# Optimization experiments

Measured on AMD Instinct MI355X. Metric: run time of the kernel, lower is better.

The kernel has to match this reference:

```python
import jax, jax.numpy as jnp
import numpy as np

B, M = 4, 4096          # events x points-per-event (row_splits are uniform)
N = B * M
IN_DIM, SPACE, PROP, K = 128, 4, 64, 32


def setup_inputs() -> dict:
    key = jax.random.key(0)
    k1, k2, k3, k4, k5 = jax.random.split(key, 5)
    x = jax.random.normal(k1, (N, IN_DIM), jnp.float32)
    row_splits = (jnp.arange(B + 1, dtype=jnp.int32) * M)
    s = 1.0 / np.sqrt(IN_DIM)
    Ws = jax.random.uniform(k2, (IN_DIM, SPACE), jnp.float32, -s, s)
    bs = jax.random.uniform(k3, (SPACE,), jnp.float32, -s, s)
    Wp = jax.random.uniform(k4, (IN_DIM, PROP), jnp.float32, -s, s)
    bp = jax.random.uniform(k5, (PROP,), jnp.float32, -s, s)
    return {"x": x, "Ws": Ws, "bs": bs, "Wp": Wp, "bp": bp, "row_splits": row_splits}


def _gravnet(x, Ws, bs, Wp, bp):
    space = x @ Ws + bs                      # [N, SPACE] learned coordinates
    prop = x @ Wp + bp                       # [N, PROP]  features to propagate
    sp = space.reshape(B, M, SPACE)
    pr = prop.reshape(B, M, PROP)
    # exact KNN within each event (row_splits segment): pairwise squared dists
    sq = jnp.sum(sp * sp, axis=-1)                         # [B, M]
    d2 = sq[:, :, None] + sq[:, None, :] - 2.0 * jnp.einsum("bms,bns->bmn", sp, sp)
    neg_vals, idx = jax.lax.top_k(-d2, K)                  # k smallest dists (incl. self)
    distsq = jnp.maximum(-neg_vals, 0.0)                   # [B, M, K]
    weights = jnp.exp(-10.0 * distsq)                      # [B, M, K]
    gathered = jax.vmap(lambda p, i: p[i])(pr, idx)        # [B, M, K, PROP]
    weighted = gathered * weights[..., None]
    fmean = jnp.mean(weighted, axis=2)                     # [B, M, PROP]
    fmax = jnp.max(weighted, axis=2)                       # [B, M, PROP]
    out = jnp.concatenate([fmean, fmax], axis=-1)          # [B, M, 2*PROP]
    return out.reshape(N, 2 * PROP)


def reference(x, Ws, bs, Wp, bp, row_splits):
    # row_splits encodes uniform segments [0, M, 2M, ...]; KNN never crosses them.
    return _gravnet(x, Ws, bs, Wp, bp)
```

## Files before the change

kernel.cpp:

```cpp
#include <hip/hip_runtime.h>
#include <hip/hip_bf16.h>
#include <math.h>

#define N_TOT   16384
#define M_EV    4096
#define IN_DIM  128
#define SPACE_D 4
#define PROP_D  64
#define K_NN    32
#define CAND_CAP 128
#define MARGIN  0.04f

typedef _Float16 h2 __attribute__((ext_vector_type(2)));
typedef unsigned long long u64;

__device__ __forceinline__ h2 pkmin(h2 a, h2 b) {
#if __has_builtin(__builtin_elementwise_min)
  return __builtin_elementwise_min(a, b);
#else
  h2 r; r.x = (a.x < b.x) ? a.x : b.x; r.y = (a.y < b.y) ? a.y : b.y; return r;
#endif
}

__device__ __forceinline__ h2 pkrtz(float a, float b) {
  return __builtin_bit_cast(h2, __builtin_amdgcn_cvt_pkrtz(a, b));
}

__global__ __launch_bounds__(256) void linear_kernel(
    const float* __restrict__ x,
    const float* __restrict__ Ws, const float* __restrict__ bs,
    const float* __restrict__ Wp, const float* __restrict__ bp,
    float* __restrict__ space, float* __restrict__ prop)
{
  const int lane = threadIdx.x & 63;
  const int wid  = threadIdx.x >> 6;
  const int r0   = __builtin_amdgcn_readfirstlane((int)blockIdx.x * 16 + wid * 4);

  const float* xr = x + (size_t)r0 * IN_DIM;

  float a0 = bp[lane];
  float a1 = a0, a2 = a0, a3 = a0;
  #pragma unroll
  for (int i = 0; i < IN_DIM; ++i) {
    const float w = Wp[i * PROP_D + lane];
    a0 = fmaf(xr[i],              w, a0);
    a1 = fmaf(xr[IN_DIM + i],     w, a1);
    a2 = fmaf(xr[2 * IN_DIM + i], w, a2);
    a3 = fmaf(xr[3 * IN_DIM + i], w, a3);
  }
  prop[(size_t)(r0 + 0) * PROP_D + lane] = a0;
  prop[(size_t)(r0 + 1) * PROP_D + lane] = a1;
  prop[(size_t)(r0 + 2) * PROP_D + lane] = a2;
  prop[(size_t)(r0 + 3) * PROP_D + lane] = a3;

  if (lane < 16) {
    const int r = lane >> 2, c = lane & 3;
    const float* xq = x + (size_t)(r0 + r) * IN_DIM;
    float a = bs[c];
    #pragma unroll
    for (int i = 0; i < IN_DIM; ++i)
      a = fmaf(xq[i], Ws[i * SPACE_D + c], a);
    space[(size_t)(r0 + r) * SPACE_D + c] = a;
  }
}

__device__ __forceinline__ int mbcnt64(u64 mk) {
  return (int)__builtin_amdgcn_mbcnt_hi((unsigned)(mk >> 32),
           __builtin_amdgcn_mbcnt_lo((unsigned)mk, 0u));
}

__global__ __launch_bounds__(512) void knn_kernel(
    const float4* __restrict__ space,
    const float*  __restrict__ prop,
    float*        __restrict__ out)
{
  const int lane = threadIdx.x & 63;
  const int wid  = threadIdx.x >> 6;
  const int row  = (int)blockIdx.x * 8 + wid;
  const int m0   = row & ~(M_EV - 1);
  const int mloc = row & (M_EV - 1);

  __shared__ uint4 s_pk[M_EV / 2];
  __shared__ int   s_ci[8][CAND_CAP];
  __shared__ uint2 s_w[8][K_NN];
  __shared__ int   s_cnt[8];

  {
    const float4* src = space + m0;
    #pragma unroll
    for (int it = 0; it < 4; ++it) {
      const int i = (int)threadIdx.x + it * 512;
      const float4 a = src[i];
      const float4 b = src[i + 2048];
      s_pk[i] = make_uint4(
        __builtin_bit_cast(unsigned, pkrtz(a.x, b.x)),
        __builtin_bit_cast(unsigned, pkrtz(a.y, b.y)),
        __builtin_bit_cast(unsigned, pkrtz(a.z, b.z)),
        __builtin_bit_cast(unsigned, pkrtz(a.w, b.w)));
    }
  }
  if (lane == 0) s_cnt[wid] = 0;
  __syncthreads();

  const float4 qf = space[m0 + mloc];
  const h2 qx = pkrtz(qf.x, qf.x), qy = pkrtz(qf.y, qf.y);
  const h2 qz = pkrtz(qf.z, qf.z), qw = pkrtz(qf.w, qf.w);

  unsigned pd[32];
  h2 mn; mn.x = (_Float16)65504.f; mn.y = (_Float16)65504.f;
  #pragma unroll
  for (int t = 0; t < 32; ++t) {
    const uint4 u = s_pk[lane + (t << 6)];
    const h2 dx = qx - __builtin_bit_cast(h2, u.x);
    const h2 dy = qy - __builtin_bit_cast(h2, u.y);
    const h2 dz = qz - __builtin_bit_cast(h2, u.z);
    const h2 dw = qw - __builtin_bit_cast(h2, u.w);
    h2 s = dx * dx;
    s = dy * dy + s;
    s = dz * dz + s;
    s = dw * dw + s;
    pd[t] = __builtin_bit_cast(unsigned, s);
    mn = pkmin(mn, s);
  }

  const float mn0 = (float)mn.x, mn1 = (float)mn.y;

  unsigned blo = 0u, bhi = 0x477FE000u;
  while (blo < bhi) {
    const unsigned mid = (blo + bhi) >> 1;
    const float fm = __uint_as_float(mid);
    const int c = (int)__popcll(__ballot(mn0 <= fm)) +
                  (int)__popcll(__ballot(mn1 <= fm));
    if (c >= K_NN) { bhi = mid; if (c == K_NN) break; }
    else blo = mid + 1;
  }
  const float T = __uint_as_float(bhi) + MARGIN;
  const h2 Th = pkrtz(T, T);

  #pragma unroll
  for (int t = 0; t < 32; ++t) {
    const h2 s = __builtin_bit_cast(h2, pd[t]);
    if (s.x <= Th.x) {
      const int pos = atomicAdd(&s_cnt[wid], 1);
      if (pos < CAND_CAP) s_ci[wid][pos] = (t << 6) + lane;
    }
    if (s.y <= Th.y) {
      const int pos = atomicAdd(&s_cnt[wid], 1);
      if (pos < CAND_CAP) s_ci[wid][pos] = (t << 6) + lane + 2048;
    }
  }
  int C = s_cnt[wid];

  if (C > CAND_CAP) {
    const float4* __restrict__ ev = space + m0;
    unsigned lo = 0u, hi = __float_as_uint(T);
    while (lo < hi) {
      const unsigned mid = (lo + hi) >> 1;
      const float fm = __uint_as_float(mid);
      int c = 0;
      #pragma unroll 1
      for (int t = 0; t < 64; ++t) {
        const float4 cc = ev[lane + (t << 6)];
        const float dx = qf.x - cc.x, dy = qf.y - cc.y;
        const float dz = qf.z - cc.z, dw = qf.w - cc.w;
        const float dd = fmaf(dx, dx, fmaf(dy, dy, fmaf(dz, dz, dw * dw)));
        c += (int)__popcll(__ballot(dd <= fm));
      }
      if (c >= K_NN) { hi = mid; if (c == K_NN) break; }
      else lo = mid + 1;
    }
    const float Tf = __uint_as_float(hi);
    int cnt = 0;
    #pragma unroll 1
    for (int pass = 0; pass < 2; ++pass) {
      #pragma unroll 1
      for (int t = 0; t < 64; ++t) {
        const float4 cc = ev[lane + (t << 6)];
        const float dx = qf.x - cc.x, dy = qf.y - cc.y;
        const float dz = qf.z - cc.z, dw = qf.w - cc.w;
        const float dd = fmaf(dx, dx, fmaf(dy, dy, fmaf(dz, dz, dw * dw)));
        const bool p = pass ? (dd == Tf) : (dd < Tf);
        const u64 mk = __ballot(p);
        if (p) {
          const int pos = cnt + mbcnt64(mk);
          if (pos < K_NN) s_ci[wid][pos] = (t << 6) + lane;
        }
        cnt += (int)__popcll(mk);
      }
      if (cnt >= K_NN) break;
    }
    C = K_NN;
  }

  const bool h0 = (lane < C), h1 = (64 + lane < C);
  const int i0 = h0 ? s_ci[wid][lane]      : 0;
  const int i1 = h1 ? s_ci[wid][64 + lane] : 0;
  float v0 = INFINITY, v1 = INFINITY;
  if (h0) {
    const float4 cc = space[m0 + i0];
    const float dx = qf.x - cc.x, dy = qf.y - cc.y;
    const float dz = qf.z - cc.z, dw = qf.w - cc.w;
    v0 = fmaf(dx, dx, fmaf(dy, dy, fmaf(dz, dz, dw * dw)));
  }
  if (h1) {
    const float4 cc = space[m0 + i1];
    const float dx = qf.x - cc.x, dy = qf.y - cc.y;
    const float dz = qf.z - cc.z, dw = qf.w - cc.w;
    v1 = fmaf(dx, dx, fmaf(dy, dy, fmaf(dz, dz, dw * dw)));
  }

  const u64 k0 = h0 ? (((u64)__float_as_uint(v0) << 12) | (unsigned)i0) : ~0ull;
  const u64 k1 = h1 ? (((u64)__float_as_uint(v1) << 12) | (unsigned)i1) : ~0ull;

  u64 klo = 0ull;
  u64 khi = (((u64)__float_as_uint(T * 1.01f + 0.02f)) << 12) | 0xFFFull;
  {
    const int c0 = (int)__popcll(__ballot(k0 <= khi)) +
                   (int)__popcll(__ballot(k1 <= khi));
    if (c0 < K_NN) khi = ((u64)0x7F800000ull << 12);
  }
  while (klo < khi) {
    const u64 mid = (klo + khi) >> 1;
    const int c = (int)__popcll(__ballot(k0 <= mid)) +
                  (int)__popcll(__ballot(k1 <= mid));
    if (c >= K_NN) { khi = mid; if (c == K_NN) break; }
    else klo = mid + 1;
  }
  const u64 Kstar = khi;

  const bool sel0 = (k0 <= Kstar), sel1 = (k1 <= Kstar);
  {
    const u64 mkS0 = __ballot(sel0);
    if (sel0) {
      const int pos = mbcnt64(mkS0);
      s_w[wid][pos] = make_uint2((unsigned)i0, __float_as_uint(__expf(-10.f * v0)));
    }
    const int b0 = (int)__popcll(mkS0);
    const u64 mkS1 = __ballot(sel1);
    if (sel1) {
      const int pos = b0 + mbcnt64(mkS1);
      s_w[wid][pos] = make_uint2((unsigned)i1, __float_as_uint(__expf(-10.f * v1)));
    }
  }

  float accm = 0.f;
  float accx = -INFINITY;
  const float* __restrict__ pb = prop + ((size_t)m0 << 6) + lane;
  #pragma unroll 8
  for (int n = 0; n < K_NN; ++n) {
    const uint2 wn = s_w[wid][n];
    const float w = __uint_as_float(wn.y);
    const float v = pb[(size_t)wn.x << 6];
    const float wv = w * v;
    accm += wv;
    accx = fmaxf(accx, wv);
  }
  out[(size_t)row * 128 + lane]      = accm * (1.f / K_NN);
  out[(size_t)row * 128 + 64 + lane] = accx;
}

extern "C" void kernel_launch(void* const* d_in, const int* in_sizes, int n_in,
                              void* d_out, int out_size, void* d_ws, size_t ws_size,
                              hipStream_t stream) {
  const float* x  = (const float*)d_in[0];
  const float* Ws = (const float*)d_in[1];
  const float* bs = (const float*)d_in[2];
  const float* Wp = (const float*)d_in[3];
  const float* bp = (const float*)d_in[4];
  float* out = (float*)d_out;

  float* prop  = (float*)d_ws;
  float* space = (float*)((char*)d_ws + (size_t)N_TOT * PROP_D * sizeof(float));

  linear_kernel<<<N_TOT / 16, 256, 0, stream>>>(x, Ws, bs, Wp, bp, space, prop);
  knn_kernel<<<N_TOT / 8, 512, 0, stream>>>((const float4*)space, prop, out);
}
```

Before: 54.87 us.

## Use fp16-bit binary search and 32-bit exact select with tie handling

The coarse threshold search now bisects directly on the 16-bit fp16 patterns of the per-lane minima, over a range of about 15 bits instead of a 32-bit float range. The exact k-selection swaps the 64-bit packed (distance, index) key bisection for a 32-bit float bisection bounded by T, and breaks ties at the threshold with ballot and mbcnt ranking. Launch bounds gain a min-blocks hint and an asm barrier pins pd in registers. This cuts iterations and 64-bit compares on the serial search path, but ties are now broken by lane order rather than by index, and the occupancy hint may force register spills.

```diff
diff --git a/kernel.cpp b/kernel.cpp
--- a/kernel.cpp
+++ b/kernel.cpp
@@ -69,7 +69,7 @@
            __builtin_amdgcn_mbcnt_lo((unsigned)mk, 0u));
 }
 
-__global__ __launch_bounds__(512) void knn_kernel(
+__global__ __launch_bounds__(512, 8) void knn_kernel(
     const float4* __restrict__ space,
     const float*  __restrict__ prop,
     float*        __restrict__ out)
@@ -123,19 +123,21 @@
     mn = pkmin(mn, s);
   }
 
-  const float mn0 = (float)mn.x, mn1 = (float)mn.y;
-
-  unsigned blo = 0u, bhi = 0x477FE000u;
+  const unsigned mnbits = __builtin_bit_cast(unsigned, mn);
+  const unsigned c0 = mnbits & 0xFFFFu, c1 = mnbits >> 16;
+  unsigned blo = 0u, bhi = 0x7C00u;
   while (blo < bhi) {
     const unsigned mid = (blo + bhi) >> 1;
-    const float fm = __uint_as_float(mid);
-    const int c = (int)__popcll(__ballot(mn0 <= fm)) +
-                  (int)__popcll(__ballot(mn1 <= fm));
+    const int c = (int)__popcll(__ballot(c0 <= mid)) +
+                  (int)__popcll(__ballot(c1 <= mid));
     if (c >= K_NN) { bhi = mid; if (c == K_NN) break; }
     else blo = mid + 1;
   }
-  const float T = __uint_as_float(bhi) + MARGIN;
+  const float T = (float)__builtin_bit_cast(_Float16, (unsigned short)bhi) + MARGIN;
   const h2 Th = pkrtz(T, T);
+
+  #pragma unroll
+  for (int t = 0; t < 32; ++t) asm volatile("" : "+v"(pd[t]));
 
   #pragma unroll
   for (int t = 0; t < 32; ++t) {
@@ -209,37 +211,40 @@
     v1 = fmaf(dx, dx, fmaf(dy, dy, fmaf(dz, dz, dw * dw)));
   }
 
-  const u64 k0 = h0 ? (((u64)__float_as_uint(v0) << 12) | (unsigned)i0) : ~0ull;
-  const u64 k1 = h1 ? (((u64)__float_as_uint(v1) << 12) | (unsigned)i1) : ~0ull;
-
-  u64 klo = 0ull;
-  u64 khi = (((u64)__float_as_uint(T * 1.01f + 0.02f)) << 12) | 0xFFFull;
-  {
-    const int c0 = (int)__popcll(__ballot(k0 <= khi)) +
-                   (int)__popcll(__ballot(k1 <= khi));
-    if (c0 < K_NN) khi = ((u64)0x7F800000ull << 12);
-  }
-  while (klo < khi) {
-    const u64 mid = (klo + khi) >> 1;
-    const int c = (int)__popcll(__ballot(k0 <= mid)) +
-                  (int)__popcll(__ballot(k1 <= mid));
-    if (c >= K_NN) { khi = mid; if (c == K_NN) break; }
-    else klo = mid + 1;
-  }
-  const u64 Kstar = khi;
-
-  const bool sel0 = (k0 <= Kstar), sel1 = (k1 <= Kstar);
+  unsigned lo = 0u, hi = __float_as_uint(T);
+  while (lo < hi) {
+    const unsigned mid = (lo + hi) >> 1;
+    const float fm = __uint_as_float(mid);
+    const int c = (int)__popcll(__ballot(v0 <= fm)) +
+                  (int)__popcll(__ballot(v1 <= fm));
+    if (c >= K_NN) { hi = mid; if (c == K_NN) break; }
+    else lo = mid + 1;
+  }
+  const float T2 = __uint_as_float(hi);
+
+  const u64 mkE0 = __ballot(v0 == T2);
+  const u64 mkE1 = __ballot(v1 == T2);
+  const int L = (int)__popcll(__ballot(v0 < T2)) +
+                (int)__popcll(__ballot(v1 < T2));
+  const int e = K_NN - L;
+  const int nE0 = (int)__popcll(mkE0);
+  const bool sel0 = (v0 < T2) || ((v0 == T2) && (mbcnt64(mkE0) < e));
+  const bool sel1 = (v1 < T2) || ((v1 == T2) && (nE0 + mbcnt64(mkE1) < e));
+
+  const float w0 = __expf(-10.f * v0);
+  const float w1 = __expf(-10.f * v1);
+
   {
     const u64 mkS0 = __ballot(sel0);
     if (sel0) {
       const int pos = mbcnt64(mkS0);
-      s_w[wid][pos] = make_uint2((unsigned)i0, __float_as_uint(__expf(-10.f * v0)));
+      s_w[wid][pos] = make_uint2((unsigned)i0, __float_as_uint(w0));
     }
     const int b0 = (int)__popcll(mkS0);
     const u64 mkS1 = __ballot(sel1);
     if (sel1) {
       const int pos = b0 + mbcnt64(mkS1);
-      s_w[wid][pos] = make_uint2((unsigned)i1, __float_as_uint(__expf(-10.f * v1)));
+      s_w[wid][pos] = make_uint2((unsigned)i1, __float_as_uint(w1));
     }
   }
 
```

Result: faster. 52.99 us (-3.4%).
